# Performance work log

Measured on AMD Instinct MI355X. Metric: run time of the kernel, lower is better.

## Reference

```python
import jax, jax.numpy as jnp
import numpy as np

E_DIM = 64  # head dim, scale = 1/sqrt(E)

def setup_inputs() -> dict:
    key = jax.random.key(0)
    k1, k2, k3 = jax.random.split(key, 3)
    B, L, H, E = 4, 2048, 8, 64
    queries = jax.random.normal(k1, (B, L, H, E), dtype=jnp.float32)
    keys = jax.random.normal(k2, (B, L, H, E), dtype=jnp.float32)
    values = jax.random.normal(k3, (B, L, H, E), dtype=jnp.float32)
    return {"queries": queries, "keys": keys, "values": values}

def reference(queries, keys, values):
    # queries: [B,L,H,E], keys: [B,S,H,E], values: [B,S,H,D]; L == S
    E = queries.shape[-1]
    scale = 1.0 / jnp.sqrt(jnp.asarray(E, dtype=queries.dtype))
    scores = jnp.einsum('blhe,bshe->bhls', queries, keys)  # [B,H,L,S]
    series = jax.nn.softmax(scale * scores, axis=-1)       # dropout p=0.0 -> identity
    V = jnp.einsum('bhls,bshd->blhd', series, values)      # [B,L,H,D]
    return V
```

## Files before the change

kernel.cpp:

```cpp
#include <hip/hip_runtime.h>

typedef __attribute__((ext_vector_type(4)))  float    f32x4;
typedef __attribute__((ext_vector_type(16))) float    f32x16;
typedef __attribute__((ext_vector_type(8)))  _Float16 half8;
typedef __attribute__((ext_vector_type(2)))  __fp16   fp16x2;
typedef __attribute__((ext_vector_type(4)))  _Float16 half4;
typedef __attribute__((ext_vector_type(8)))  short    short8;

#define SCL2E 0.18033688011112042f

__device__ __forceinline__ unsigned short f2h_bits(float x) {
    union { _Float16 h; unsigned short u; } c;
    c.h = (_Float16)x;
    return c.u;
}

__device__ __forceinline__ void gl_lds16(const unsigned short* g, unsigned short* l) {
    __builtin_amdgcn_global_load_lds((const __attribute__((address_space(1))) void*)g,
                                     (__attribute__((address_space(3))) void*)l, 16, 0, 0);
}

__global__ __launch_bounds__(256)
void cvt_kv_kernel(const float* __restrict__ K, const float* __restrict__ V,
                   unsigned short* __restrict__ wsK, unsigned short* __restrict__ wsV) {
    int bid = blockIdx.x;
    if (bid < 4096) {
        int t   = bid * 256 + threadIdx.x;
        int eg  = t & 15;
        int gr  = t >> 4;
        int row = gr & 2047, bh = gr >> 11;
        int b = bh >> 3, h = bh & 7;
        const float* sp = K + (((size_t)b * 2048 + row) * 8 + h) * 64 + eg * 4;
        f32x4 v = *(const f32x4*)sp;
        int cg = (eg & ~3) | ((eg & 1) << 1) | ((eg >> 1) & 1);
        cg ^= (row & 7) << 1;
        union { unsigned short s[4]; unsigned long long u; } o;
        o.s[0] = f2h_bits(v[0]); o.s[1] = f2h_bits(v[1]);
        o.s[2] = f2h_bits(v[2]); o.s[3] = f2h_bits(v[3]);
        *(unsigned long long*)(wsK + (size_t)gr * 64 + cg * 4) = o.u;
    } else {
        int t   = (bid - 4096) * 256 + threadIdx.x;
        int d   = t & 63;
        int g   = t >> 6;
        int kv4 = g & 511, bh = g >> 9;
        int b = bh >> 3, h = bh & 7;
        int kv = kv4 * 4;
        const float* sp = V + (((size_t)b * 2048 + kv) * 8 + h) * 64 + d;
        float v0 = sp[0], v1 = sp[512], v2 = sp[1024], v3 = sp[1536];
        int lg  = kv4 & 15;
        int lgp = (lg & ~3) | ((lg & 1) << 1) | ((lg >> 1) & 1);
        lgp ^= (d & 7) << 1;
        union { unsigned short s[4]; unsigned long long u; } o;
        o.s[0] = f2h_bits(v0); o.s[1] = f2h_bits(v1);
        o.s[2] = f2h_bits(v2); o.s[3] = f2h_bits(v3);
        *(unsigned long long*)(wsV + ((size_t)bh * 64 + d) * 2048 + (kv4 & ~15) * 4 + lgp * 4) = o.u;
    }
}

__global__ __launch_bounds__(512, 4)
void attn_v4_kernel(const float* __restrict__ Q,
                    const unsigned short* __restrict__ wsK,
                    const unsigned short* __restrict__ wsV,
                    float* __restrict__ O) {
    __shared__ __align__(16) unsigned short lds[2][2][2][4096];
    __shared__ __align__(16) unsigned short lds_q[128 * 64];

    const int tid  = threadIdx.x;
    const int lane = tid & 63;
    const int w    = tid >> 6;
    const int qw   = w & 3;
    const int kh   = w >> 2;
    const int lq   = lane & 31;
    const int hi   = lane >> 5;
    const int swz  = (lq & 7) << 3;

    const int bid = blockIdx.x;
    const int xcd = bid & 7, slot = bid >> 3;
    const int qt  = slot & 15;
    const int bh  = ((slot >> 4) << 3) | xcd;
    const int q0  = qt * 128;
    const int b   = bh >> 3, h = bh & 7;

    const unsigned short* Ksrc = wsK + (size_t)bh * 2048 * 64;
    const unsigned short* Vsrc = wsV + (size_t)bh * 64 * 2048;
    float* Og = O + ((size_t)b * 2048 * 8 + (size_t)h) * 64;

#pragma unroll
    for (int p = 0; p < 4; ++p) {
        int t  = tid + 512 * p;
        int eg = t & 15;
        int r  = t >> 4;
        const float* sp = Q + (((size_t)b * 2048 + q0 + r) * 8 + h) * 64 + eg * 4;
        f32x4 v = *(const f32x4*)sp;
        int cg = (eg & ~3) | ((eg & 1) << 1) | ((eg >> 1) & 1);
        cg ^= (r & 7) << 1;
        union { unsigned short s[4]; unsigned long long u; } o;
        o.s[0] = f2h_bits(v[0] * SCL2E); o.s[1] = f2h_bits(v[1] * SCL2E);
        o.s[2] = f2h_bits(v[2] * SCL2E); o.s[3] = f2h_bits(v[3] * SCL2E);
        *(unsigned long long*)&lds_q[r * 64 + cg * 4] = o.u;
    }

    {
        const size_t kvb0 = 0, kvb1 = 1024;
        gl_lds16(Ksrc + kvb0 * 64 + tid * 8, &lds[0][0][0][tid * 8]);
        gl_lds16(Vsrc + (size_t)(tid >> 3) * 2048 + kvb0 + (tid & 7) * 8, &lds[0][1][0][tid * 8]);
        gl_lds16(Ksrc + kvb1 * 64 + tid * 8, &lds[0][0][1][tid * 8]);
        gl_lds16(Vsrc + (size_t)(tid >> 3) * 2048 + kvb1 + (tid & 7) * 8, &lds[0][1][1][tid * 8]);
    }
    __syncthreads();

    int off[4];
#pragma unroll
    for (int ks = 0; ks < 4; ++ks) off[ks] = (ks * 16 + hi * 8) ^ swz;

    half8 qf[4];
    {
        int qrow = qw * 32 + lq;
#pragma unroll
        for (int ks = 0; ks < 4; ++ks)
            qf[ks] = *(const half8*)&lds_q[qrow * 64 + off[ks]];
    }

    f32x16 acc0 = {0.f,0.f,0.f,0.f,0.f,0.f,0.f,0.f,0.f,0.f,0.f,0.f,0.f,0.f,0.f,0.f};
    f32x16 acc1 = acc0;
    float lrowA = 0.f, lrowB = 0.f;
    const fp16x2 vone = {(__fp16)1.0f, (__fp16)1.0f};

    for (int t = 0; t < 16; ++t) {
        const int cur = t & 1;
        if (t + 1 < 16) {
            const int nxt = cur ^ 1;
            const size_t kv0 = (size_t)(t + 1) * 64;
            const size_t kvb0 = kv0, kvb1 = 1024 + kv0;
            gl_lds16(Ksrc + kvb0 * 64 + tid * 8, &lds[nxt][0][0][tid * 8]);
            gl_lds16(Vsrc + (size_t)(tid >> 3) * 2048 + kvb0 + (tid & 7) * 8, &lds[nxt][1][0][tid * 8]);
            gl_lds16(Ksrc + kvb1 * 64 + tid * 8, &lds[nxt][0][1][tid * 8]);
            gl_lds16(Vsrc + (size_t)(tid >> 3) * 2048 + kvb1 + (tid & 7) * 8, &lds[nxt][1][1][tid * 8]);
        }

        const unsigned short* kb = &lds[cur][0][kh][0];
        f32x16 s0 = {0.f,0.f,0.f,0.f,0.f,0.f,0.f,0.f,0.f,0.f,0.f,0.f,0.f,0.f,0.f,0.f};
        f32x16 s1 = s0;
        __builtin_amdgcn_s_setprio(1);
#pragma unroll
        for (int ks = 0; ks < 4; ++ks) {
            half8 kf0 = *(const half8*)&kb[lq * 64 + off[ks]];
            half8 kf1 = *(const half8*)&kb[(32 + lq) * 64 + off[ks]];
            s0 = __builtin_amdgcn_mfma_f32_32x32x16_f16(kf0, qf[ks], s0, 0, 0, 0);
            s1 = __builtin_amdgcn_mfma_f32_32x32x16_f16(kf1, qf[ks], s1, 0, 0, 0);
        }
        __builtin_amdgcn_s_setprio(0);

        half8 pf[4];
        float pA = 0.f, pB = 0.f;
#pragma unroll
        for (int hm = 0; hm < 2; ++hm) {
            const f32x16& sb = hm ? s1 : s0;
#pragma unroll
            for (int hk = 0; hk < 2; ++hk) {
                union { fp16x2 h2[4]; half8 v; } u;
#pragma unroll
                for (int j = 0; j < 4; ++j) {
                    float e0 = __builtin_amdgcn_exp2f(sb[8 * hk + 2 * j]);
                    float e1 = __builtin_amdgcn_exp2f(sb[8 * hk + 2 * j + 1]);
                    u.h2[j] = __builtin_amdgcn_cvt_pkrtz(e0, e1);
#if __has_builtin(__builtin_amdgcn_fdot2)
                    if (hm == 0) pA = __builtin_amdgcn_fdot2(u.h2[j], vone, pA, false);
                    else         pB = __builtin_amdgcn_fdot2(u.h2[j], vone, pB, false);
#else
                    if (hm == 0) pA += e0 + e1; else pB += e0 + e1;
#endif
                }
                pf[2 * hm + hk] = u.v;
            }
        }
        lrowA += pA; lrowB += pB;

        const unsigned short* vb = &lds[cur][1][kh][0];
        __builtin_amdgcn_s_setprio(1);
#pragma unroll
        for (int kc = 0; kc < 4; ++kc) {
            half8 vf0 = *(const half8*)&vb[lq * 64 + off[kc]];
            half8 vf1 = *(const half8*)&vb[(32 + lq) * 64 + off[kc]];
            acc0 = __builtin_amdgcn_mfma_f32_32x32x16_f16(vf0, pf[kc], acc0, 0, 0, 0);
            acc1 = __builtin_amdgcn_mfma_f32_32x32x16_f16(vf1, pf[kc], acc1, 0, 0, 0);
        }
        __builtin_amdgcn_s_setprio(0);

        __syncthreads();
    }

    float lrow = lrowA + lrowB;
    lrow += __shfl_xor(lrow, 32);

    float* mlds = (float*)&lds[0][0][0][0];
    const int mslot = (qw * 64 + lane) * 36;
    if (kh) {
        float* dst = mlds + mslot;
#pragma unroll
        for (int a = 0; a < 4; ++a) {
            *(f32x4*)(dst + 4 * a)      = (f32x4){acc0[4*a], acc0[4*a+1], acc0[4*a+2], acc0[4*a+3]};
            *(f32x4*)(dst + 16 + 4 * a) = (f32x4){acc1[4*a], acc1[4*a+1], acc1[4*a+2], acc1[4*a+3]};
        }
        dst[32] = lrow;
    }
    __syncthreads();
    if (!kh) {
        const float* src = mlds + mslot;
        float inv = 1.0f / (lrow + src[32]);

        const int qg = q0 + qw * 32 + lq;
        float* orow = Og + (size_t)qg * 512;
#pragma unroll
        for (int a = 0; a < 4; ++a) {
            f32x4 p0 = *(const f32x4*)(src + 4 * a);
            f32x4 p1 = *(const f32x4*)(src + 16 + 4 * a);
            f32x4 o0, o1;
#pragma unroll
            for (int i = 0; i < 4; ++i) {
                o0[i] = (acc0[4 * a + i] + p0[i]) * inv;
                o1[i] = (acc1[4 * a + i] + p1[i]) * inv;
            }
            *(f32x4*)(orow + 8 * a + 4 * hi)      = o0;
            *(f32x4*)(orow + 32 + 8 * a + 4 * hi) = o1;
        }
    }
}

__device__ __forceinline__ unsigned short f2bf(float f) {
    union { float f; unsigned u; } v; v.f = f;
    unsigned u = v.u;
    u += 0x7fffu + ((u >> 16) & 1u);
    return (unsigned short)(u >> 16);
}

__global__ __launch_bounds__(128, 2)
void attn_v1_kernel(const float* __restrict__ Q, const float* __restrict__ K,
                    const float* __restrict__ V, float* __restrict__ O) {
    __shared__ __align__(16) unsigned short lds_q[64 * 64];
    __shared__ __align__(16) unsigned short lds_k[64 * 64];
    __shared__ __align__(16) unsigned short lds_v[64 * 64];

    const int tid = threadIdx.x, lane = tid & 63, wv = tid >> 6;
    const int lq = lane & 15, g = lane >> 4;
    const int bid = blockIdx.x, xcd = bid & 7, slot = bid >> 3;
    const int qt = slot & 31;
    const int bh = ((slot >> 5) << 3) | xcd;
    const int b = bh >> 3, h = bh & 7;
    const size_t base = ((size_t)b * 2048 * 8 + (size_t)h) * 64;
    const float* Qg = Q + base; const float* Kg = K + base;
    const float* Vg = V + base; float* Og = O + base;
    const int q0 = qt * 64;
    const float S2E = 0.125f * 1.44269504088896341f;

#pragma unroll
    for (int p = 0; p < 16; ++p) {
        int r = (tid >> 5) + p * 4, e = (tid & 31) * 2;
        const float* src = Qg + (size_t)(q0 + r) * 512 + e;
        unsigned pk = (unsigned)f2bf(src[0]) | ((unsigned)f2bf(src[1]) << 16);
        *(unsigned*)&lds_q[(r * 64 + e) ^ ((r & 7) << 3)] = pk;
    }
    __syncthreads();
    short8 qf[2][2];
#pragma unroll
    for (int qc = 0; qc < 2; ++qc) {
        int row = wv * 32 + qc * 16 + lq;
#pragma unroll
        for (int j = 0; j < 2; ++j)
            qf[qc][j] = *(const short8*)&lds_q[(row * 64 + j * 32 + g * 8) ^ ((row & 7) << 3)];
    }
    f32x4 acc[2][4];
#pragma unroll
    for (int qc = 0; qc < 2; ++qc)
#pragma unroll
        for (int dc = 0; dc < 4; ++dc) acc[qc][dc] = (f32x4){0.f, 0.f, 0.f, 0.f};
    float mrow[2] = {-1e30f, -1e30f}, lrow[2] = {0.f, 0.f};

    for (int t = 0; t < 32; ++t) {
        const int kv0 = t * 64;
        __syncthreads();
#pragma unroll
        for (int p = 0; p < 16; ++p) {
            int r = (tid >> 5) + p * 4, e = (tid & 31) * 2;
            const float* src = Kg + (size_t)(kv0 + r) * 512 + e;
            unsigned pk = (unsigned)f2bf(src[0]) | ((unsigned)f2bf(src[1]) << 16);
            *(unsigned*)&lds_k[(r * 64 + e) ^ ((r & 7) << 3)] = pk;
        }
#pragma unroll
        for (int p = 0; p < 16; ++p) {
            int d = tid & 63, kv = (p * 2 + (tid >> 6)) * 2;
            float v0 = Vg[(size_t)(kv0 + kv) * 512 + d];
            float v1 = Vg[(size_t)(kv0 + kv + 1) * 512 + d];
            union { _Float16 hh[2]; unsigned u; } pk;
            pk.hh[0] = (_Float16)v0; pk.hh[1] = (_Float16)v1;
            *(unsigned*)&lds_v[(d * 64 + kv) ^ ((d & 15) << 2)] = pk.u;
        }
        __syncthreads();
        f32x4 sfr[2][4];
#pragma unroll
        for (int kc = 0; kc < 4; ++kc) {
            int row = kc * 16 + lq;
            short8 kf0 = *(const short8*)&lds_k[(row * 64 + 0 + g * 8) ^ ((row & 7) << 3)];
            short8 kf1 = *(const short8*)&lds_k[(row * 64 + 32 + g * 8) ^ ((row & 7) << 3)];
#pragma unroll
            for (int qc = 0; qc < 2; ++qc) {
                f32x4 s = __builtin_amdgcn_mfma_f32_16x16x32_bf16(kf0, qf[qc][0], (f32x4){0.f,0.f,0.f,0.f}, 0, 0, 0);
                s = __builtin_amdgcn_mfma_f32_16x16x32_bf16(kf1, qf[qc][1], s, 0, 0, 0);
                sfr[qc][kc] = s;
            }
        }
        half4 pfv[2][4];
#pragma unroll
        for (int qc = 0; qc < 2; ++qc) {
            float smax = -1e30f;
#pragma unroll
            for (int kc = 0; kc < 4; ++kc)
#pragma unroll
                for (int r = 0; r < 4; ++r) smax = fmaxf(smax, sfr[qc][kc][r]);
            smax = fmaxf(smax, __shfl_xor(smax, 16));
            smax = fmaxf(smax, __shfl_xor(smax, 32));
            float mn = fmaxf(mrow[qc], smax);
            float alpha = __builtin_amdgcn_exp2f((mrow[qc] - mn) * S2E);
            mrow[qc] = mn;
            float msc = mn * S2E, psum = 0.f;
#pragma unroll
            for (int kc = 0; kc < 4; ++kc)
#pragma unroll
                for (int r = 0; r < 4; ++r) {
                    float p = __builtin_amdgcn_exp2f(sfr[qc][kc][r] * S2E - msc);
                    psum += p;
                    pfv[qc][kc][r] = (_Float16)p;
                }
            psum += __shfl_xor(psum, 16);
            psum += __shfl_xor(psum, 32);
            lrow[qc] = lrow[qc] * alpha + psum;
#pragma unroll
            for (int dc = 0; dc < 4; ++dc) acc[qc][dc] *= alpha;
        }
#pragma unroll
        for (int dc = 0; dc < 4; ++dc) {
            int dd = dc * 16 + lq;
#pragma unroll
            for (int kc = 0; kc < 4; ++kc) {
                half4 vf = *(const half4*)&lds_v[(dd * 64 + kc * 16 + g * 4) ^ ((dd & 15) << 2)];
                acc[0][dc] = __builtin_amdgcn_mfma_f32_16x16x16f16(vf, pfv[0][kc], acc[0][dc], 0, 0, 0);
                acc[1][dc] = __builtin_amdgcn_mfma_f32_16x16x16f16(vf, pfv[1][kc], acc[1][dc], 0, 0, 0);
            }
        }
    }
#pragma unroll
    for (int qc = 0; qc < 2; ++qc) {
        float inv = 1.f / lrow[qc];
        int qrow = q0 + wv * 32 + qc * 16 + lq;
#pragma unroll
        for (int dc = 0; dc < 4; ++dc) {
            f32x4 o = acc[qc][dc] * inv;
            *(f32x4*)(Og + (size_t)qrow * 512 + dc * 16 + g * 4) = o;
        }
    }
}

extern "C" void kernel_launch(void* const* d_in, const int* in_sizes, int n_in,
                              void* d_out, int out_size, void* d_ws, size_t ws_size,
                              hipStream_t stream) {
    const float* Q = (const float*)d_in[0];
    const float* K = (const float*)d_in[1];
    const float* V = (const float*)d_in[2];
    float* O = (float*)d_out;

    const size_t per = (size_t)32 * 2048 * 64;
    const size_t need = 2 * per * sizeof(unsigned short);
    if (ws_size >= need) {
        unsigned short* wsK = (unsigned short*)d_ws;
        unsigned short* wsV = wsK + per;
        cvt_kv_kernel<<<dim3(8192), dim3(256), 0, stream>>>(K, V, wsK, wsV);
        attn_v4_kernel<<<dim3(512), dim3(512), 0, stream>>>(Q, wsK, wsV, O);
    } else {
        attn_v1_kernel<<<dim3(1024), dim3(128), 0, stream>>>(Q, K, V, O);
    }
}
```

Baseline: 59.01 us.

## Repack K/V workspace into tile-contiguous rows with 16-way XOR swizzle

The conversion kernel now writes K and V half-precision tiles so that each 64-key tile is one contiguous 8 KB block. Rows are paired, so each LDS row is 128 elements holding both 32-row halves, with an XOR swizzle over 16 granules. Global-to-LDS loads become straight contiguous copies instead of strided V gathers. The wider swizzle is meant to reduce LDS bank conflicts on MFMA operand reads. The risk is index-mapping mistakes and a more costly scattered write pattern in the conversion kernel.

```diff
diff --git a/kernel.cpp b/kernel.cpp
--- a/kernel.cpp
+++ b/kernel.cpp
@@ -28,16 +28,18 @@
         int t   = bid * 256 + threadIdx.x;
         int eg  = t & 15;
         int gr  = t >> 4;
-        int row = gr & 2047, bh = gr >> 11;
+        int kv  = gr & 2047, bh = gr >> 11;
         int b = bh >> 3, h = bh & 7;
-        const float* sp = K + (((size_t)b * 2048 + row) * 8 + h) * 64 + eg * 4;
+        const float* sp = K + (((size_t)b * 2048 + kv) * 8 + h) * 64 + eg * 4;
         f32x4 v = *(const f32x4*)sp;
-        int cg = (eg & ~3) | ((eg & 1) << 1) | ((eg >> 1) & 1);
-        cg ^= (row & 7) << 1;
+        int T = kv >> 6, R = kv & 31, half = (kv >> 5) & 1;
+        int egp = (eg & ~3) | ((eg & 1) << 1) | ((eg >> 1) & 1);
+        int gnl = (half * 8 + (egp >> 1)) ^ (R & 15);
+        size_t idx = (((size_t)bh * 32 + T) * 32 + R) * 128 + gnl * 8 + (egp & 1) * 4;
         union { unsigned short s[4]; unsigned long long u; } o;
         o.s[0] = f2h_bits(v[0]); o.s[1] = f2h_bits(v[1]);
         o.s[2] = f2h_bits(v[2]); o.s[3] = f2h_bits(v[3]);
-        *(unsigned long long*)(wsK + (size_t)gr * 64 + cg * 4) = o.u;
+        *(unsigned long long*)(wsK + idx) = o.u;
     } else {
         int t   = (bid - 4096) * 256 + threadIdx.x;
         int d   = t & 63;
@@ -47,18 +49,20 @@
         int kv = kv4 * 4;
         const float* sp = V + (((size_t)b * 2048 + kv) * 8 + h) * 64 + d;
         float v0 = sp[0], v1 = sp[512], v2 = sp[1024], v3 = sp[1536];
-        int lg  = kv4 & 15;
-        int lgp = (lg & ~3) | ((lg & 1) << 1) | ((lg >> 1) & 1);
-        lgp ^= (d & 7) << 1;
+        int T = kv >> 6, R = d & 31, halfd = d >> 5;
+        int kvg  = (kv >> 2) & 15;
+        int kvgp = (kvg & ~3) | ((kvg & 1) << 1) | ((kvg >> 1) & 1);
+        int gnl  = (halfd * 8 + (kvgp >> 1)) ^ (R & 15);
+        size_t idx = (((size_t)bh * 32 + T) * 32 + R) * 128 + gnl * 8 + (kvgp & 1) * 4;
         union { unsigned short s[4]; unsigned long long u; } o;
         o.s[0] = f2h_bits(v0); o.s[1] = f2h_bits(v1);
         o.s[2] = f2h_bits(v2); o.s[3] = f2h_bits(v3);
-        *(unsigned long long*)(wsV + ((size_t)bh * 64 + d) * 2048 + (kv4 & ~15) * 4 + lgp * 4) = o.u;
+        *(unsigned long long*)(wsV + idx) = o.u;
     }
 }
 
 __global__ __launch_bounds__(512, 4)
-void attn_v4_kernel(const float* __restrict__ Q,
+void attn_v6_kernel(const float* __restrict__ Q,
                     const unsigned short* __restrict__ wsK,
                     const unsigned short* __restrict__ wsV,
                     float* __restrict__ O) {
@@ -72,7 +76,6 @@
     const int kh   = w >> 2;
     const int lq   = lane & 31;
     const int hi   = lane >> 5;
-    const int swz  = (lq & 7) << 3;
 
     const int bid = blockIdx.x;
     const int xcd = bid & 7, slot = bid >> 3;
@@ -81,8 +84,8 @@
     const int q0  = qt * 128;
     const int b   = bh >> 3, h = bh & 7;
 
-    const unsigned short* Ksrc = wsK + (size_t)bh * 2048 * 64;
-    const unsigned short* Vsrc = wsV + (size_t)bh * 64 * 2048;
+    const unsigned short* Ksrc = wsK + (size_t)bh * 32 * 4096;
+    const unsigned short* Vsrc = wsV + (size_t)bh * 32 * 4096;
     float* Og = O + ((size_t)b * 2048 * 8 + (size_t)h) * 64;
 
 #pragma unroll
@@ -101,24 +104,28 @@
     }
 
     {
-        const size_t kvb0 = 0, kvb1 = 1024;
-        gl_lds16(Ksrc + kvb0 * 64 + tid * 8, &lds[0][0][0][tid * 8]);
-        gl_lds16(Vsrc + (size_t)(tid >> 3) * 2048 + kvb0 + (tid & 7) * 8, &lds[0][1][0][tid * 8]);
-        gl_lds16(Ksrc + kvb1 * 64 + tid * 8, &lds[0][0][1][tid * 8]);
-        gl_lds16(Vsrc + (size_t)(tid >> 3) * 2048 + kvb1 + (tid & 7) * 8, &lds[0][1][1][tid * 8]);
+        gl_lds16(Ksrc + (size_t)0  * 4096 + tid * 8, &lds[0][0][0][tid * 8]);
+        gl_lds16(Vsrc + (size_t)0  * 4096 + tid * 8, &lds[0][1][0][tid * 8]);
+        gl_lds16(Ksrc + (size_t)16 * 4096 + tid * 8, &lds[0][0][1][tid * 8]);
+        gl_lds16(Vsrc + (size_t)16 * 4096 + tid * 8, &lds[0][1][1][tid * 8]);
     }
     __syncthreads();
 
-    int off[4];
-#pragma unroll
-    for (int ks = 0; ks < 4; ++ks) off[ks] = (ks * 16 + hi * 8) ^ swz;
+    int of0[4], of1[4];
+#pragma unroll
+    for (int ks = 0; ks < 4; ++ks) {
+        of0[ks] = (((ks * 2 + hi)     ^ (lq & 15)) << 3);
+        of1[ks] = (((8 + ks * 2 + hi) ^ (lq & 15)) << 3);
+    }
 
     half8 qf[4];
     {
         int qrow = qw * 32 + lq;
 #pragma unroll
-        for (int ks = 0; ks < 4; ++ks)
-            qf[ks] = *(const half8*)&lds_q[qrow * 64 + off[ks]];
+        for (int ks = 0; ks < 4; ++ks) {
+            int offQ = (ks * 16 + hi * 8) ^ ((lq & 7) << 3);
+            qf[ks] = *(const half8*)&lds_q[qrow * 64 + offQ];
+        }
     }
 
     f32x16 acc0 = {0.f,0.f,0.f,0.f,0.f,0.f,0.f,0.f,0.f,0.f,0.f,0.f,0.f,0.f,0.f,0.f};
@@ -130,12 +137,10 @@
         const int cur = t & 1;
         if (t + 1 < 16) {
             const int nxt = cur ^ 1;
-            const size_t kv0 = (size_t)(t + 1) * 64;
-            const size_t kvb0 = kv0, kvb1 = 1024 + kv0;
-            gl_lds16(Ksrc + kvb0 * 64 + tid * 8, &lds[nxt][0][0][tid * 8]);
-            gl_lds16(Vsrc + (size_t)(tid >> 3) * 2048 + kvb0 + (tid & 7) * 8, &lds[nxt][1][0][tid * 8]);
-            gl_lds16(Ksrc + kvb1 * 64 + tid * 8, &lds[nxt][0][1][tid * 8]);
-            gl_lds16(Vsrc + (size_t)(tid >> 3) * 2048 + kvb1 + (tid & 7) * 8, &lds[nxt][1][1][tid * 8]);
+            gl_lds16(Ksrc + (size_t)(t + 1)  * 4096 + tid * 8, &lds[nxt][0][0][tid * 8]);
+            gl_lds16(Vsrc + (size_t)(t + 1)  * 4096 + tid * 8, &lds[nxt][1][0][tid * 8]);
+            gl_lds16(Ksrc + (size_t)(t + 17) * 4096 + tid * 8, &lds[nxt][0][1][tid * 8]);
+            gl_lds16(Vsrc + (size_t)(t + 17) * 4096 + tid * 8, &lds[nxt][1][1][tid * 8]);
         }
 
         const unsigned short* kb = &lds[cur][0][kh][0];
@@ -144,8 +149,8 @@
         __builtin_amdgcn_s_setprio(1);
 #pragma unroll
         for (int ks = 0; ks < 4; ++ks) {
-            half8 kf0 = *(const half8*)&kb[lq * 64 + off[ks]];
-            half8 kf1 = *(const half8*)&kb[(32 + lq) * 64 + off[ks]];
+            half8 kf0 = *(const half8*)&kb[lq * 128 + of0[ks]];
+            half8 kf1 = *(const half8*)&kb[lq * 128 + of1[ks]];
             s0 = __builtin_amdgcn_mfma_f32_32x32x16_f16(kf0, qf[ks], s0, 0, 0, 0);
             s1 = __builtin_amdgcn_mfma_f32_32x32x16_f16(kf1, qf[ks], s1, 0, 0, 0);
         }
@@ -180,8 +185,8 @@
         __builtin_amdgcn_s_setprio(1);
 #pragma unroll
         for (int kc = 0; kc < 4; ++kc) {
-            half8 vf0 = *(const half8*)&vb[lq * 64 + off[kc]];
-            half8 vf1 = *(const half8*)&vb[(32 + lq) * 64 + off[kc]];
+            half8 vf0 = *(const half8*)&vb[lq * 128 + of0[kc]];
+            half8 vf1 = *(const half8*)&vb[lq * 128 + of1[kc]];
             acc0 = __builtin_amdgcn_mfma_f32_32x32x16_f16(vf0, pf[kc], acc0, 0, 0, 0);
             acc1 = __builtin_amdgcn_mfma_f32_32x32x16_f16(vf1, pf[kc], acc1, 0, 0, 0);
         }
@@ -374,7 +379,7 @@
         unsigned short* wsK = (unsigned short*)d_ws;
         unsigned short* wsV = wsK + per;
         cvt_kv_kernel<<<dim3(8192), dim3(256), 0, stream>>>(K, V, wsK, wsV);
-        attn_v4_kernel<<<dim3(512), dim3(512), 0, stream>>>(Q, wsK, wsV, O);
+        attn_v6_kernel<<<dim3(512), dim3(512), 0, stream>>>(Q, wsK, wsV, O);
     } else {
         attn_v1_kernel<<<dim3(1024), dim3(128), 0, stream>>>(Q, K, V, O);
     }
```

Result: no change. 58.51 us (-0.8%).
